# Kernel optimization log

Hardware: AMD Instinct MI355X
Metric: run time of the kernel (lower is better)

Reference implementation:

```python
import jax, jax.numpy as jnp
import numpy as np

NUM_CLASSES = 256
N_ITERS = 25  # fixed Lloyd iterations (sklearn default max_iter=300; fixed count for a jit-able reference)


def setup_inputs() -> dict:
    key = jax.random.key(0)
    k1, k2 = jax.random.split(key)
    features = jax.random.normal(k1, (65536, 1024), dtype=jnp.float32)
    logits = jax.random.normal(k2, (65536, 256), dtype=jnp.float32)
    return {"features": features, "logits": logits}


def _segment_mean_centroids(features, labels, num_classes, prev_centroids):
    # scatter-mean of features into per-class centroids; keep previous centroid if a class is empty
    sums = jax.ops.segment_sum(features, labels, num_segments=num_classes)      # [C, D]
    counts = jax.ops.segment_sum(jnp.ones((features.shape[0],), features.dtype),
                                 labels, num_segments=num_classes)               # [C]
    has = counts > 0
    means = sums / jnp.maximum(counts, 1.0)[:, None]
    return jnp.where(has[:, None], means, prev_centroids)


def _assign(features, centroids):
    # argmin of squared euclidean distance; ||x||^2 term is constant per row, drop it
    # scores[n, c] = -2 x_n . mu_c + ||mu_c||^2
    scores = -2.0 * jnp.einsum('nd,cd->nc', features, centroids) + jnp.sum(centroids * centroids, axis=1)[None, :]
    return jnp.argmin(scores, axis=1)


def reference(features, logits):
    # KMeans.forward: labels = argmax(logits); centroids init from label centers (centroid_init='label_centers');
    # then Lloyd's k-means (sklearn KMeans with init=centroids, n_init=1) and return cluster labels.
    init_labels = jnp.argmax(logits, axis=1)
    # get_centroids: empty classes stay at zero
    zeros = jnp.zeros((NUM_CLASSES, features.shape[1]), features.dtype)
    centroids = _segment_mean_centroids(features, init_labels, NUM_CLASSES, zeros)

    def body(i, centroids):
        labels = _assign(features, centroids)
        return _segment_mean_centroids(features, labels, NUM_CLASSES, centroids)

    centroids = jax.lax.fori_loop(0, N_ITERS, body, centroids)
    pseudo_labels = _assign(features, centroids)
    return pseudo_labels.astype(jnp.int64)
```

## Files before the change

kernel.cpp:

```cpp
#include <hip/hip_runtime.h>

#define N_PTS 65536
#define DIM   1024
#define NCLS  256
#define NITER 25

typedef __attribute__((ext_vector_type(8)))  short short8;
typedef __attribute__((ext_vector_type(16))) float f32x16;

__device__ __forceinline__ unsigned short bf_split(float x, float& rem) {
    unsigned u = __float_as_uint(x);
    unsigned b = (u + 0x7fffu + ((u >> 16) & 1u)) & 0xffff0000u;
    rem = x - __uint_as_float(b);
    return (unsigned short)(b >> 16);
}
__device__ __forceinline__ unsigned short bf_rne(float x) {
    unsigned u = __float_as_uint(x);
    return (unsigned short)((u + 0x7fffu + ((u >> 16) & 1u)) >> 16);
}

__device__ __forceinline__ void gload_lds16(const void* g, void* l) {
    __builtin_amdgcn_global_load_lds(
        (const __attribute__((address_space(1))) unsigned int*)g,
        (__attribute__((address_space(3))) unsigned int*)l, 16, 0, 0);
}

__global__ void k_argmax(const float* __restrict__ logits, int* __restrict__ labels) {
    int row  = blockIdx.x * 4 + (threadIdx.x >> 6);
    int lane = threadIdx.x & 63;
    float4 v = reinterpret_cast<const float4*>(logits + (size_t)row * NCLS)[lane];
    float bv = v.x; int bi = lane * 4;
    if (v.y > bv) { bv = v.y; bi = lane * 4 + 1; }
    if (v.z > bv) { bv = v.z; bi = lane * 4 + 2; }
    if (v.w > bv) { bv = v.w; bi = lane * 4 + 3; }
    #pragma unroll
    for (int off = 32; off >= 1; off >>= 1) {
        float ov = __shfl_down(bv, off, 64);
        int   oi = __shfl_down(bi, off, 64);
        if (ov > bv || (ov == bv && oi < bi)) { bv = ov; bi = oi; }
    }
    if (lane == 0) labels[row] = bi;
}

__global__ void k_hist(const int* __restrict__ labels, int* __restrict__ counts) {
    __shared__ int h[NCLS];
    h[threadIdx.x] = 0;
    __syncthreads();
    for (int i = blockIdx.x * blockDim.x + threadIdx.x; i < N_PTS;
         i += gridDim.x * blockDim.x)
        atomicAdd(&h[labels[i]], 1);
    __syncthreads();
    int v = h[threadIdx.x];
    if (v) atomicAdd(&counts[threadIdx.x], v);
}

__global__ __launch_bounds__(512) void k_accum(const float* __restrict__ feat,
                                               const int* __restrict__ labels,
                                               float* __restrict__ partials) {
    __shared__ unsigned long long s[NCLS * 32];
    int tid = threadIdx.x;
    for (int i = tid; i < NCLS * 32; i += 512) s[i] = 0ull;
    __syncthreads();
    int slice = blockIdx.x;
    int chunk = blockIdx.y;
    int w = tid >> 6, l = tid & 63;
    int sub = l >> 3;
    int dq  = l & 7;
    const size_t dbase = (size_t)slice * 32 + dq * 4;
    for (int step = 0; step < 128; ++step) {
        int p = chunk * 8192 + step * 64 + w * 8 + sub;
        int c = labels[p];
        float4 f = *reinterpret_cast<const float4*>(feat + (size_t)p * DIM + dbase);
        unsigned long long* dst = &s[c * 32 + dq * 4];
        atomicAdd(dst + 0, (unsigned long long)__double2ll_rn((double)f.x * 16777216.0));
        atomicAdd(dst + 1, (unsigned long long)__double2ll_rn((double)f.y * 16777216.0));
        atomicAdd(dst + 2, (unsigned long long)__double2ll_rn((double)f.z * 16777216.0));
        atomicAdd(dst + 3, (unsigned long long)__double2ll_rn((double)f.w * 16777216.0));
    }
    __syncthreads();
    float* out = partials + (size_t)chunk * NCLS * DIM;
    for (int i = tid; i < NCLS * 32; i += 512) {
        int c = i >> 5, d = i & 31;
        out[(size_t)c * DIM + slice * 32 + d] =
            (float)((double)(long long)s[i] * (1.0 / 16777216.0));
    }
}

__global__ void k_final(const float* __restrict__ partials,
                        const int* __restrict__ counts,
                        float* __restrict__ centroids,
                        float* __restrict__ norms,
                        unsigned short* __restrict__ Bs) {
    int c = blockIdx.x, t = threadIdx.x;
    size_t off = ((size_t)c * 256 + t) * 4;
    float4 sum = make_float4(0.f, 0.f, 0.f, 0.f);
    for (int ch = 0; ch < 8; ++ch) {
        float4 p = *reinterpret_cast<const float4*>(partials + (size_t)ch * NCLS * DIM + off);
        sum.x += p.x; sum.y += p.y; sum.z += p.z; sum.w += p.w;
    }
    int cnt = counts[c];
    float4 outv;
    if (cnt > 0) {
        float fc = (float)cnt;
        outv = make_float4(sum.x / fc, sum.y / fc, sum.z / fc, sum.w / fc);
    } else {
        outv = *reinterpret_cast<const float4*>(centroids + off);
    }
    *reinterpret_cast<float4*>(centroids + off) = outv;

    float s = outv.x * outv.x + outv.y * outv.y + outv.z * outv.z + outv.w * outv.w;
    __shared__ float red[4];
    #pragma unroll
    for (int o = 32; o >= 1; o >>= 1) s += __shfl_down(s, o, 64);
    if ((t & 63) == 0) red[t >> 6] = s;
    __syncthreads();
    if (t == 0) norms[c] = red[0] + red[1] + red[2] + red[3];

    int k = t * 4;
    int kc = k >> 5, kh = (k >> 4) & 1, jg = (k >> 3) & 1, j0 = k & 7;
    int nt = c >> 5, lane = (c & 31) + 32 * jg;
    float xv[4] = {outv.x, outv.y, outv.z, outv.w};
    unsigned short hv[4], mv[4], lv[4];
    #pragma unroll
    for (int e = 0; e < 4; ++e) {
        float r1, r2;
        hv[e] = bf_split(xv[e], r1);
        mv[e] = bf_split(r1, r2);
        lv[e] = bf_rne(r2);
    }
    #pragma unroll
    for (int p = 0; p < 3; ++p) {
        size_t base = ((((size_t)kc * 3 + p) * 8 + nt) * 2 + kh) * 512 + (size_t)lane * 8 + j0;
        const unsigned short* sp = (p == 0) ? hv : (p == 1) ? mv : lv;
        *reinterpret_cast<uint2*>(&Bs[base]) = *reinterpret_cast<const uint2*>(sp);
    }
}

__global__ __launch_bounds__(256, 2) void k_assign(
        const float* __restrict__ feat, const unsigned short* __restrict__ Bs,
        const float* __restrict__ norms, int* __restrict__ counts,
        int* __restrict__ out_labels) {
    __shared__ __align__(16) unsigned short Bl[3 * 16 * 512];
    __shared__ int h[NCLS];
    int tid = threadIdx.x, w = tid >> 6, l = tid & 63;
    int cn = l & 31, jg = l >> 5;
    int p0 = blockIdx.x * 128;
    h[tid] = 0;

    f32x16 acc[8];
    #pragma unroll
    for (int t = 0; t < 8; ++t)
        #pragma unroll
        for (int i = 0; i < 16; ++i) acc[t][i] = 0.f;

    const float* arow = feat + (size_t)(p0 + w * 32 + cn) * DIM + jg * 8;

    union AF { short8 v; unsigned short u[8]; } af[2][3];
    float4 ga0, ga1, ga2, ga3;

    auto issue_b = [&](int kc_, int q_, int rb_) {
        #pragma unroll
        for (int i = 0; i < 4; ++i) {
            int s = w * 4 + i;
            const unsigned short* g = Bs +
                ((((size_t)kc_ * 3 + q_) * 8 + (s >> 1)) * 2 + (s & 1)) * 512 +
                (size_t)l * 8;
            gload_lds16(g, &Bl[(rb_ * 16 + s) * 512]);
        }
    };
    auto load_a = [&](int kc_) {
        const float* ab = arow + kc_ * 32;
        asm volatile("global_load_dwordx4 %0, %1, off"           : "=v"(ga0) : "v"(ab) : "memory");
        asm volatile("global_load_dwordx4 %0, %1, off offset:16" : "=v"(ga1) : "v"(ab) : "memory");
        asm volatile("global_load_dwordx4 %0, %1, off offset:64" : "=v"(ga2) : "v"(ab) : "memory");
        asm volatile("global_load_dwordx4 %0, %1, off offset:80" : "=v"(ga3) : "v"(ab) : "memory");
    };
    auto split_a = [&]() {
        float xs[16] = {ga0.x, ga0.y, ga0.z, ga0.w, ga1.x, ga1.y, ga1.z, ga1.w,
                        ga2.x, ga2.y, ga2.z, ga2.w, ga3.x, ga3.y, ga3.z, ga3.w};
        #pragma unroll
        for (int kh = 0; kh < 2; ++kh)
            #pragma unroll
            for (int j = 0; j < 8; ++j) {
                float r1, r2;
                af[kh][0].u[j] = bf_split(xs[kh * 8 + j], r1);
                af[kh][1].u[j] = bf_split(r1, r2);
                af[kh][2].u[j] = bf_rne(r2);
            }
    };
    auto mfma_phase = [&](int rb, int np) {
        #pragma unroll
        for (int kh = 0; kh < 2; ++kh) {
            short8 bf[8];
            #pragma unroll
            for (int ntl = 0; ntl < 8; ++ntl)
                bf[ntl] = *reinterpret_cast<const short8*>(
                    &Bl[(rb * 16 + ntl * 2 + kh) * 512 + l * 8]);
            #pragma unroll
            for (int p = 0; p < 3; ++p)
                if (p < np) {
                    #pragma unroll
                    for (int ntl = 0; ntl < 8; ++ntl)
                        acc[ntl] = __builtin_amdgcn_mfma_f32_32x32x16_bf16(
                            af[kh][p].v, bf[ntl], acc[ntl], 0, 0, 0);
                }
        }
    };

    issue_b(0, 0, 0);
    load_a(0);
    issue_b(0, 1, 1);
    asm volatile("s_waitcnt vmcnt(4)" ::: "memory");
    __builtin_amdgcn_sched_barrier(0);
    split_a();

    for (int kc = 0; kc < 32; ++kc) {
        const bool lastk = (kc == 31);
        asm volatile("s_waitcnt vmcnt(4)" ::: "memory");
        __builtin_amdgcn_s_barrier();
        issue_b(kc, 2, 2);
        __builtin_amdgcn_s_setprio(1);
        mfma_phase(0, 3);
        __builtin_amdgcn_s_setprio(0);
        asm volatile("s_waitcnt vmcnt(4)" ::: "memory");
        __builtin_amdgcn_s_barrier();
        if (!lastk) {
            issue_b(kc + 1, 0, 0);
            load_a(kc + 1);
        }
        __builtin_amdgcn_s_setprio(1);
        mfma_phase(1, 2);
        __builtin_amdgcn_s_setprio(0);
        if (!lastk) { asm volatile("s_waitcnt vmcnt(8)" ::: "memory"); }
        else        { asm volatile("s_waitcnt vmcnt(0)" ::: "memory"); }
        __builtin_amdgcn_s_barrier();
        if (!lastk) {
            issue_b(kc + 1, 1, 1);
            asm volatile("s_waitcnt vmcnt(4)" ::: "memory");
            __builtin_amdgcn_sched_barrier(0);
        }
        __builtin_amdgcn_s_setprio(1);
        mfma_phase(2, 1);
        __builtin_amdgcn_s_setprio(0);
        if (!lastk) split_a();
    }

    float nrm[8];
    #pragma unroll
    for (int ntl = 0; ntl < 8; ++ntl) nrm[ntl] = norms[ntl * 32 + cn];
    #pragma unroll
    for (int r = 0; r < 16; ++r) {
        unsigned long long key = ~0ull;
        #pragma unroll
        for (int ntl = 0; ntl < 8; ++ntl) {
            float s = nrm[ntl] - 2.0f * acc[ntl][r];
            unsigned u = __float_as_uint(s);
            u = (u & 0x80000000u) ? ~u : (u | 0x80000000u);
            unsigned long long kk =
                ((unsigned long long)u << 32) | (unsigned)(ntl * 32 + cn);
            key = (kk < key) ? kk : key;
        }
        #pragma unroll
        for (int off = 16; off >= 1; off >>= 1) {
            unsigned long long ok = __shfl_xor(key, off, 64);
            key = (ok < key) ? ok : key;
        }
        if (cn == 0) {
            int m = p0 + w * 32 + (r & 3) + 8 * (r >> 2) + 4 * jg;
            int lab = (int)(key & 0xffffffffull);
            out_labels[m] = lab;
            atomicAdd(&h[lab], 1);
        }
    }
    __syncthreads();
    int v = h[tid];
    if (v) atomicAdd(&counts[tid], v);
}

extern "C" void kernel_launch(void* const* d_in, const int* in_sizes, int n_in,
                              void* d_out, int out_size, void* d_ws, size_t ws_size,
                              hipStream_t stream) {
    const float* feat   = (const float*)d_in[0];
    const float* logits = (const float*)d_in[1];
    int* out_labels = (int*)d_out;

    char* ws = (char*)d_ws;
    float* centroids            = (float*)ws;
    float* partials             = (float*)(ws + 0x100000);
    float* norms                = (float*)(ws + 0x900000);
    int*   counts               = (int*)  (ws + 0x901000);
    int*   labels               = (int*)  (ws + 0x902000);
    unsigned short* Bs          = (unsigned short*)(ws + 0x950000);

    k_argmax<<<N_PTS / 4, 256, 0, stream>>>(logits, labels);
    hipMemsetAsync(centroids, 0, (size_t)NCLS * DIM * sizeof(float), stream);
    hipMemsetAsync(counts, 0, NCLS * sizeof(int), stream);
    k_hist<<<64, 256, 0, stream>>>(labels, counts);
    k_accum<<<dim3(32, 8), 512, 0, stream>>>(feat, labels, partials);
    k_final<<<NCLS, 256, 0, stream>>>(partials, counts, centroids, norms, Bs);

    for (int it = 0; it < NITER; ++it) {
        hipMemsetAsync(counts, 0, NCLS * sizeof(int), stream);
        k_assign<<<N_PTS / 128, 256, 0, stream>>>(feat, Bs, norms, counts, labels);
        k_accum<<<dim3(32, 8), 512, 0, stream>>>(feat, labels, partials);
        k_final<<<NCLS, 256, 0, stream>>>(partials, counts, centroids, norms, Bs);
    }

    k_assign<<<N_PTS / 128, 256, 0, stream>>>(feat, Bs, norms, counts, out_labels);
}
```

Measured before the change: 7.269 ms.

## Read centroid fragments directly from global memory instead of staging through LDS

Drops the LDS-staged, barrier-synchronised, hand-pipelined path that fed centroid B fragments via global_load_lds. Each wave now loads its B fragments straight from global memory (served from L2, since every block reads them) and keeps a simple register double-buffer for the feature A rows. This removes the LDS footprint, the block barriers and the manual waitcnt scheduling. The cost is that each of the four waves fetches the same B data from global memory with no explicit overlap, so MFMA issue may stall on memory latency.

```diff
diff --git a/kernel.cpp b/kernel.cpp
--- a/kernel.cpp
+++ b/kernel.cpp
@@ -17,12 +17,6 @@
 __device__ __forceinline__ unsigned short bf_rne(float x) {
     unsigned u = __float_as_uint(x);
     return (unsigned short)((u + 0x7fffu + ((u >> 16) & 1u)) >> 16);
-}
-
-__device__ __forceinline__ void gload_lds16(const void* g, void* l) {
-    __builtin_amdgcn_global_load_lds(
-        (const __attribute__((address_space(1))) unsigned int*)g,
-        (__attribute__((address_space(3))) unsigned int*)l, 16, 0, 0);
 }
 
 __global__ void k_argmax(const float* __restrict__ logits, int* __restrict__ labels) {
@@ -140,12 +134,12 @@
         const float* __restrict__ feat, const unsigned short* __restrict__ Bs,
         const float* __restrict__ norms, int* __restrict__ counts,
         int* __restrict__ out_labels) {
-    __shared__ __align__(16) unsigned short Bl[3 * 16 * 512];
     __shared__ int h[NCLS];
     int tid = threadIdx.x, w = tid >> 6, l = tid & 63;
     int cn = l & 31, jg = l >> 5;
     int p0 = blockIdx.x * 128;
     h[tid] = 0;
+    __syncthreads();
 
     f32x16 acc[8];
     #pragma unroll
@@ -155,29 +149,15 @@
 
     const float* arow = feat + (size_t)(p0 + w * 32 + cn) * DIM + jg * 8;
 
-    union AF { short8 v; unsigned short u[8]; } af[2][3];
-    float4 ga0, ga1, ga2, ga3;
-
-    auto issue_b = [&](int kc_, int q_, int rb_) {
-        #pragma unroll
-        for (int i = 0; i < 4; ++i) {
-            int s = w * 4 + i;
-            const unsigned short* g = Bs +
-                ((((size_t)kc_ * 3 + q_) * 8 + (s >> 1)) * 2 + (s & 1)) * 512 +
-                (size_t)l * 8;
-            gload_lds16(g, &Bl[(rb_ * 16 + s) * 512]);
-        }
-    };
-    auto load_a = [&](int kc_) {
-        const float* ab = arow + kc_ * 32;
-        asm volatile("global_load_dwordx4 %0, %1, off"           : "=v"(ga0) : "v"(ab) : "memory");
-        asm volatile("global_load_dwordx4 %0, %1, off offset:16" : "=v"(ga1) : "v"(ab) : "memory");
-        asm volatile("global_load_dwordx4 %0, %1, off offset:64" : "=v"(ga2) : "v"(ab) : "memory");
-        asm volatile("global_load_dwordx4 %0, %1, off offset:80" : "=v"(ga3) : "v"(ab) : "memory");
-    };
-    auto split_a = [&]() {
-        float xs[16] = {ga0.x, ga0.y, ga0.z, ga0.w, ga1.x, ga1.y, ga1.z, ga1.w,
-                        ga2.x, ga2.y, ga2.z, ga2.w, ga3.x, ga3.y, ga3.z, ga3.w};
+    float4 cur0 = *reinterpret_cast<const float4*>(arow);
+    float4 cur1 = *reinterpret_cast<const float4*>(arow + 4);
+    float4 cur2 = *reinterpret_cast<const float4*>(arow + 16);
+    float4 cur3 = *reinterpret_cast<const float4*>(arow + 20);
+
+    for (int kc = 0; kc < 32; ++kc) {
+        float xs[16] = {cur0.x, cur0.y, cur0.z, cur0.w, cur1.x, cur1.y, cur1.z, cur1.w,
+                        cur2.x, cur2.y, cur2.z, cur2.w, cur3.x, cur3.y, cur3.z, cur3.w};
+        union { short8 v; unsigned short u[8]; } af[2][3];
         #pragma unroll
         for (int kh = 0; kh < 2; ++kh)
             #pragma unroll
@@ -187,62 +167,33 @@
                 af[kh][1].u[j] = bf_split(r1, r2);
                 af[kh][2].u[j] = bf_rne(r2);
             }
-    };
-    auto mfma_phase = [&](int rb, int np) {
-        #pragma unroll
-        for (int kh = 0; kh < 2; ++kh) {
-            short8 bf[8];
+        if (kc < 31) {
+            const float* ab = arow + (kc + 1) * 32;
+            cur0 = *reinterpret_cast<const float4*>(ab);
+            cur1 = *reinterpret_cast<const float4*>(ab + 4);
+            cur2 = *reinterpret_cast<const float4*>(ab + 16);
+            cur3 = *reinterpret_cast<const float4*>(ab + 20);
+        }
+        const unsigned short* bkc = Bs + (size_t)kc * 24576 + (size_t)l * 8;
+        #pragma unroll
+        for (int q = 0; q < 3; ++q)
             #pragma unroll
-            for (int ntl = 0; ntl < 8; ++ntl)
-                bf[ntl] = *reinterpret_cast<const short8*>(
-                    &Bl[(rb * 16 + ntl * 2 + kh) * 512 + l * 8]);
-            #pragma unroll
-            for (int p = 0; p < 3; ++p)
-                if (p < np) {
-                    #pragma unroll
-                    for (int ntl = 0; ntl < 8; ++ntl)
-                        acc[ntl] = __builtin_amdgcn_mfma_f32_32x32x16_bf16(
-                            af[kh][p].v, bf[ntl], acc[ntl], 0, 0, 0);
-                }
-        }
-    };
-
-    issue_b(0, 0, 0);
-    load_a(0);
-    issue_b(0, 1, 1);
-    asm volatile("s_waitcnt vmcnt(4)" ::: "memory");
-    __builtin_amdgcn_sched_barrier(0);
-    split_a();
-
-    for (int kc = 0; kc < 32; ++kc) {
-        const bool lastk = (kc == 31);
-        asm volatile("s_waitcnt vmcnt(4)" ::: "memory");
-        __builtin_amdgcn_s_barrier();
-        issue_b(kc, 2, 2);
-        __builtin_amdgcn_s_setprio(1);
-        mfma_phase(0, 3);
-        __builtin_amdgcn_s_setprio(0);
-        asm volatile("s_waitcnt vmcnt(4)" ::: "memory");
-        __builtin_amdgcn_s_barrier();
-        if (!lastk) {
-            issue_b(kc + 1, 0, 0);
-            load_a(kc + 1);
-        }
-        __builtin_amdgcn_s_setprio(1);
-        mfma_phase(1, 2);
-        __builtin_amdgcn_s_setprio(0);
-        if (!lastk) { asm volatile("s_waitcnt vmcnt(8)" ::: "memory"); }
-        else        { asm volatile("s_waitcnt vmcnt(0)" ::: "memory"); }
-        __builtin_amdgcn_s_barrier();
-        if (!lastk) {
-            issue_b(kc + 1, 1, 1);
-            asm volatile("s_waitcnt vmcnt(4)" ::: "memory");
-            __builtin_amdgcn_sched_barrier(0);
-        }
-        __builtin_amdgcn_s_setprio(1);
-        mfma_phase(2, 1);
-        __builtin_amdgcn_s_setprio(0);
-        if (!lastk) split_a();
+            for (int kh = 0; kh < 2; ++kh) {
+                short8 bf[8];
+                #pragma unroll
+                for (int ntl = 0; ntl < 8; ++ntl)
+                    bf[ntl] = *reinterpret_cast<const short8*>(
+                        bkc + ((q * 8 + ntl) * 2 + kh) * 512);
+                const int np = (q == 0) ? 3 : (q == 1) ? 2 : 1;
+                #pragma unroll
+                for (int p = 0; p < 3; ++p)
+                    if (p < np) {
+                        #pragma unroll
+                        for (int ntl = 0; ntl < 8; ++ntl)
+                            acc[ntl] = __builtin_amdgcn_mfma_f32_32x32x16_bf16(
+                                af[kh][p].v, bf[ntl], acc[ntl], 0, 0, 0);
+                    }
+            }
     }
 
     float nrm[8];
```

Measured after the change: 7.508 ms. 3.3% more time.
